# Kernel optimization log

Measured on AMD Instinct MI355X. Metric: run time of the kernel, lower is better.

Reference implementation:

```python
import jax, jax.numpy as jnp
import numpy as np

B, N, CI, CO = 2, 64, 32, 32  # batch, n points, Rs_in channels (j), Rs_out channels (i)


def setup_inputs() -> dict:
    key = jax.random.key(0)
    kf, kg, kw = jax.random.split(key, 3)
    features = jax.random.normal(kf, (B, N, N, CI), dtype=jnp.float32)
    geometry = jax.random.normal(kg, (B, N, 3), dtype=jnp.float32)
    # Continuous kernel parameters: linear map from relative vector (xyz) to 6*CO*CI kernel entries
    W = jax.random.normal(kw, (3, 6 * CO * CI), dtype=jnp.float32) / jnp.sqrt(3.0)
    return {"features": features, "geometry": geometry, "W": W, "n_norm": 1}


def reference(features, geometry, W, n_norm):
    z, n = geometry.shape[:2]
    ci = features.shape[-1]
    co = W.shape[1] // (6 * ci)
    # rel[z, a, b] = r_b - r_a  (rb = unsqueeze(1), ra = unsqueeze(2))
    rel = geometry[:, None, :, :] - geometry[:, :, None, :]  # [z, a, b, 3]
    k = jnp.einsum('zabx,xk->zabk', rel, W).reshape(z, n, n, 6 * co, ci)
    k = k / jnp.sqrt(6.0 * (n_norm ** 2))
    k1, k2, k3, k4, k5, k6 = jnp.split(k, 6, axis=3)  # each [z, a, b, i, j]
    # Precompute shared feature reductions over c and d once (fused HBM savings)
    fs = features.sum(axis=2)   # sum over d -> [z, c, j]
    fd = features.sum(axis=1)   # sum over c -> [z, d, j]
    ft = fs.sum(axis=1)         # sum over c,d -> [z, j]
    out = jnp.einsum('zabij,zj->zabi', k1, ft)
    out = out + jnp.einsum('zacij,zcj->zai', k2, fs)[:, :, None, :]
    out = out + jnp.einsum('zadij,zdj->zai', k3, fd)[:, :, None, :]
    out = out + jnp.einsum('zbcij,zcj->zbi', k4, fs)[:, None, :, :]
    out = out + jnp.einsum('zbdij,zdj->zbi', k5, fd)[:, None, :, :]
    out = out + jnp.einsum('zcdij,zcdj->zi', k6, features)[:, None, None, :]
    return out  # [z, a, b, i]
```

## Files before the change

### kernel.cpp

```cpp
#include <hip/hip_runtime.h>
#include <math.h>

#define NZ 2
#define NN 64
#define NCI 32
#define NCO 32
#define NBZ 32
#define NROWS (4096 / NBZ)

__device__ __forceinline__ void ld4(const float* __restrict__ p, float* d) {
    const float4 v = *(const float4*)p;
    d[0] = v.x; d[1] = v.y; d[2] = v.z; d[3] = v.w;
}

__global__ __launch_bounds__(256) void k_single(const float* __restrict__ feat,
                                                const float* __restrict__ geom,
                                                const float* __restrict__ W,
                                                const int* __restrict__ nnp,
                                                float* __restrict__ out) {
    const int bid = blockIdx.x;
    const int z   = bid >> 5;
    const int s   = bid & 31;
    const int tid = threadIdx.x;
    const int wv  = tid >> 6;
    const int lane = tid & 63;
    const int rg  = tid >> 3;
    const int cg  = tid & 7;

    __shared__ float gsh[NN * 3];
    __shared__ float wred[4][7][32];
    __shared__ float sacc[7][32];
    __shared__ float gred[3][32];
    __shared__ float stab[224];

    if (tid < NN * 3) gsh[tid] = geom[z * NN * 3 + tid];
    __syncthreads();

    float ft[4] = {0.f, 0.f, 0.f, 0.f};
    float Gs[3][4] = {{0.f}};
    float Gd[3][4] = {{0.f}};
    const float* fz = feat + (size_t)z * 4096 * NCI;
    #pragma unroll
    for (int rr = 0; rr < 2; ++rr) {
        const int c = rg * 2 + rr;
        const float gc0 = gsh[c * 3 + 0], gc1 = gsh[c * 3 + 1], gc2 = gsh[c * 3 + 2];
        const float* rowp = fz + (size_t)c * 64 * NCI + cg * 4;
        float rs[4] = {0.f, 0.f, 0.f, 0.f};
        #pragma unroll 4
        for (int d = 0; d < 64; ++d) {
            float f[4];
            ld4(rowp + d * NCI, f);
            const float gd0 = gsh[d * 3 + 0], gd1 = gsh[d * 3 + 1], gd2 = gsh[d * 3 + 2];
            #pragma unroll
            for (int k = 0; k < 4; ++k) {
                rs[k] += f[k];
                Gd[0][k] = fmaf(gd0, f[k], Gd[0][k]);
                Gd[1][k] = fmaf(gd1, f[k], Gd[1][k]);
                Gd[2][k] = fmaf(gd2, f[k], Gd[2][k]);
            }
        }
        #pragma unroll
        for (int k = 0; k < 4; ++k) {
            ft[k] += rs[k];
            Gs[0][k] = fmaf(gc0, rs[k], Gs[0][k]);
            Gs[1][k] = fmaf(gc1, rs[k], Gs[1][k]);
            Gs[2][k] = fmaf(gc2, rs[k], Gs[2][k]);
        }
    }

    float v[7][4];
    #pragma unroll
    for (int k = 0; k < 4; ++k) {
        v[0][k] = ft[k];
        #pragma unroll
        for (int x = 0; x < 3; ++x) { v[1 + x][k] = Gs[x][k]; v[4 + x][k] = Gd[x][k]; }
    }
    #pragma unroll
    for (int q = 0; q < 7; ++q)
        #pragma unroll
        for (int k = 0; k < 4; ++k) {
            float t = v[q][k];
            t += __shfl_xor(t, 8);
            t += __shfl_xor(t, 16);
            t += __shfl_xor(t, 32);
            v[q][k] = t;
        }
    if (lane < 8) {
        #pragma unroll
        for (int q = 0; q < 7; ++q)
            #pragma unroll
            for (int k = 0; k < 4; ++k) wred[wv][q][lane * 4 + k] = v[q][k];
    }
    __syncthreads();
    if (tid < 224) {
        const int q = tid >> 5, j = tid & 31;
        sacc[q][j] = wred[0][q][j] + wred[1][q][j] + wred[2][q][j] + wred[3][q][j];
    }
    __syncthreads();

    const int vn = *nnp;
    const float nnv = (vn > 0 && vn < (1 << 23)) ? (float)vn : __int_as_float(vn);
    const float scale = 1.0f / sqrtf(6.0f * nnv * nnv);

    if (tid < 96) {
        const int x = tid >> 5, i = tid & 31;
        const float* Wp = W + x * 6 * NCO * NCI + i * NCI;
        float q1 = 0.f, q23 = 0.f, q45 = 0.f, gp = 0.f;
        #pragma unroll 2
        for (int j4 = 0; j4 < 8; ++j4) {
            float w[6][4];
            #pragma unroll
            for (int m = 0; m < 6; ++m) ld4(Wp + m * 1024 + j4 * 4, w[m]);
            #pragma unroll
            for (int k = 0; k < 4; ++k) {
                const int j = j4 * 4 + k;
                const float ftj = sacc[0][j];
                const float gsj = sacc[1 + x][j];
                const float gdj = sacc[4 + x][j];
                q1  = fmaf(w[0][k], ftj, q1);
                q23 = fmaf(w[1][k] + w[2][k], ftj, q23);
                q45 = fmaf(w[3][k] + w[4][k], ftj, q45);
                gp  = fmaf(w[1][k] + w[3][k] - w[5][k], gsj, gp);
                gp  = fmaf(w[2][k] + w[4][k] + w[5][k], gdj, gp);
            }
        }
        stab[tid]      = scale * (q1 + q23);
        stab[96 + tid] = scale * (q1 - q45);
        gred[x][i] = gp;
    }
    __syncthreads();
    if (tid < 32) stab[192 + tid] = scale * (gred[0][tid] + gred[1][tid] + gred[2][tid]);
    __syncthreads();

    const int i0 = cg * 4;
    float qa[3][4], qb[3][4], gm[4];
    #pragma unroll
    for (int k = 0; k < 4; ++k) gm[k] = stab[192 + i0 + k];
    #pragma unroll
    for (int x = 0; x < 3; ++x)
        #pragma unroll
        for (int k = 0; k < 4; ++k) {
            qa[x][k] = stab[x * 32 + i0 + k];
            qb[x][k] = stab[96 + x * 32 + i0 + k];
        }

    #pragma unroll
    for (int u = 0; u < 4; ++u) {
        const int pr = rg + u * 32;
        const int ab = s * NROWS + pr;
        const int a = ab >> 6, b = ab & 63;
        float r[4];
        #pragma unroll
        for (int k = 0; k < 4; ++k) r[k] = gm[k];
        #pragma unroll
        for (int x = 0; x < 3; ++x) {
            const float gb = gsh[b * 3 + x], ga = gsh[a * 3 + x];
            #pragma unroll
            for (int k = 0; k < 4; ++k)
                r[k] = fmaf(gb, qb[x][k], fmaf(-ga, qa[x][k], r[k]));
        }
        float4 o; o.x = r[0]; o.y = r[1]; o.z = r[2]; o.w = r[3];
        *(float4*)(out + ((size_t)(z * 4096 + ab)) * 32 + i0) = o;
    }
}

extern "C" void kernel_launch(void* const* d_in, const int* in_sizes, int n_in,
                              void* d_out, int out_size, void* d_ws, size_t ws_size,
                              hipStream_t stream) {
    const float* feat = (const float*)d_in[0];
    const float* geom = (const float*)d_in[1];
    const float* W    = (const float*)d_in[2];
    const int*   nnp  = (const int*)d_in[3];

    k_single<<<NZ * NBZ, 256, 0, stream>>>(feat, geom, W, nnp, (float*)d_out);
}
```

Before: 16.81 us.

## Widen blocks to 1024 threads and redistribute reduction, weight and output work

Raises the block size from 256 to 1024 threads. Each thread now reduces half of one feature row, the W contraction is split across 8 lanes per output and combined with shuffles, and each thread writes one output vector instead of four. The goal is to shorten each thread's serial chain and expose more memory parallelism in a latency-bound redundant reduction that every block repeats. The cost is a larger 16-wave cross-wave reduction, more shuffles, and possibly lower occupancy or register pressure at 1024 threads per block.

```diff
diff --git a/kernel.cpp b/kernel.cpp
--- a/kernel.cpp
+++ b/kernel.cpp
@@ -6,29 +6,26 @@
 #define NCI 32
 #define NCO 32
 #define NBZ 32
-#define NROWS (4096 / NBZ)
 
 __device__ __forceinline__ void ld4(const float* __restrict__ p, float* d) {
     const float4 v = *(const float4*)p;
     d[0] = v.x; d[1] = v.y; d[2] = v.z; d[3] = v.w;
 }
 
-__global__ __launch_bounds__(256) void k_single(const float* __restrict__ feat,
-                                                const float* __restrict__ geom,
-                                                const float* __restrict__ W,
-                                                const int* __restrict__ nnp,
-                                                float* __restrict__ out) {
-    const int bid = blockIdx.x;
-    const int z   = bid >> 5;
-    const int s   = bid & 31;
-    const int tid = threadIdx.x;
-    const int wv  = tid >> 6;
+__global__ __launch_bounds__(1024) void k_single(const float* __restrict__ feat,
+                                                 const float* __restrict__ geom,
+                                                 const float* __restrict__ W,
+                                                 const int* __restrict__ nnp,
+                                                 float* __restrict__ out) {
+    const int bid  = blockIdx.x;
+    const int z    = bid >> 5;
+    const int s    = bid & 31;
+    const int tid  = threadIdx.x;
     const int lane = tid & 63;
-    const int rg  = tid >> 3;
-    const int cg  = tid & 7;
+    const int wv   = tid >> 6;
 
     __shared__ float gsh[NN * 3];
-    __shared__ float wred[4][7][32];
+    __shared__ float wred[16][7][32];
     __shared__ float sacc[7][32];
     __shared__ float gred[3][32];
     __shared__ float stab[224];
@@ -36,44 +33,35 @@
     if (tid < NN * 3) gsh[tid] = geom[z * NN * 3 + tid];
     __syncthreads();
 
-    float ft[4] = {0.f, 0.f, 0.f, 0.f};
-    float Gs[3][4] = {{0.f}};
+    const int cg = tid & 7;
+    const int dh = (tid >> 3) & 1;
+    const int c  = tid >> 4;
+    const float gc0 = gsh[c * 3 + 0], gc1 = gsh[c * 3 + 1], gc2 = gsh[c * 3 + 2];
+
+    float rs[4] = {0.f, 0.f, 0.f, 0.f};
     float Gd[3][4] = {{0.f}};
-    const float* fz = feat + (size_t)z * 4096 * NCI;
-    #pragma unroll
-    for (int rr = 0; rr < 2; ++rr) {
-        const int c = rg * 2 + rr;
-        const float gc0 = gsh[c * 3 + 0], gc1 = gsh[c * 3 + 1], gc2 = gsh[c * 3 + 2];
-        const float* rowp = fz + (size_t)c * 64 * NCI + cg * 4;
-        float rs[4] = {0.f, 0.f, 0.f, 0.f};
-        #pragma unroll 4
-        for (int d = 0; d < 64; ++d) {
-            float f[4];
-            ld4(rowp + d * NCI, f);
-            const float gd0 = gsh[d * 3 + 0], gd1 = gsh[d * 3 + 1], gd2 = gsh[d * 3 + 2];
-            #pragma unroll
-            for (int k = 0; k < 4; ++k) {
-                rs[k] += f[k];
-                Gd[0][k] = fmaf(gd0, f[k], Gd[0][k]);
-                Gd[1][k] = fmaf(gd1, f[k], Gd[1][k]);
-                Gd[2][k] = fmaf(gd2, f[k], Gd[2][k]);
-            }
-        }
+    const float* rowp = feat + ((size_t)z * 4096 + c * 64 + dh * 32) * NCI + cg * 4;
+    #pragma unroll 8
+    for (int t = 0; t < 32; ++t) {
+        float f[4];
+        ld4(rowp + t * NCI, f);
+        const int d = dh * 32 + t;
+        const float gd0 = gsh[d * 3 + 0], gd1 = gsh[d * 3 + 1], gd2 = gsh[d * 3 + 2];
         #pragma unroll
         for (int k = 0; k < 4; ++k) {
-            ft[k] += rs[k];
-            Gs[0][k] = fmaf(gc0, rs[k], Gs[0][k]);
-            Gs[1][k] = fmaf(gc1, rs[k], Gs[1][k]);
-            Gs[2][k] = fmaf(gc2, rs[k], Gs[2][k]);
+            rs[k] += f[k];
+            Gd[0][k] = fmaf(gd0, f[k], Gd[0][k]);
+            Gd[1][k] = fmaf(gd1, f[k], Gd[1][k]);
+            Gd[2][k] = fmaf(gd2, f[k], Gd[2][k]);
         }
     }
 
     float v[7][4];
     #pragma unroll
     for (int k = 0; k < 4; ++k) {
-        v[0][k] = ft[k];
-        #pragma unroll
-        for (int x = 0; x < 3; ++x) { v[1 + x][k] = Gs[x][k]; v[4 + x][k] = Gd[x][k]; }
+        v[0][k] = rs[k];
+        v[1][k] = gc0 * rs[k]; v[2][k] = gc1 * rs[k]; v[3][k] = gc2 * rs[k];
+        v[4][k] = Gd[0][k];    v[5][k] = Gd[1][k];    v[6][k] = Gd[2][k];
     }
     #pragma unroll
     for (int q = 0; q < 7; ++q)
@@ -94,7 +82,10 @@
     __syncthreads();
     if (tid < 224) {
         const int q = tid >> 5, j = tid & 31;
-        sacc[q][j] = wred[0][q][j] + wred[1][q][j] + wred[2][q][j] + wred[3][q][j];
+        float sum = 0.f;
+        #pragma unroll
+        for (int g = 0; g < 16; ++g) sum += wred[g][q][j];
+        sacc[q][j] = sum;
     }
     __syncthreads();
 
@@ -102,66 +93,59 @@
     const float nnv = (vn > 0 && vn < (1 << 23)) ? (float)vn : __int_as_float(vn);
     const float scale = 1.0f / sqrtf(6.0f * nnv * nnv);
 
-    if (tid < 96) {
-        const int x = tid >> 5, i = tid & 31;
-        const float* Wp = W + x * 6 * NCO * NCI + i * NCI;
+    if (tid < 768) {
+        const int x = tid >> 8, i = (tid >> 3) & 31, jg = tid & 7;
+        const float* Wp = W + x * 6 * NCO * NCI + i * NCI + jg * 4;
+        float w[6][4];
+        #pragma unroll
+        for (int m = 0; m < 6; ++m) ld4(Wp + m * 1024, w[m]);
         float q1 = 0.f, q23 = 0.f, q45 = 0.f, gp = 0.f;
-        #pragma unroll 2
-        for (int j4 = 0; j4 < 8; ++j4) {
-            float w[6][4];
-            #pragma unroll
-            for (int m = 0; m < 6; ++m) ld4(Wp + m * 1024 + j4 * 4, w[m]);
-            #pragma unroll
-            for (int k = 0; k < 4; ++k) {
-                const int j = j4 * 4 + k;
-                const float ftj = sacc[0][j];
-                const float gsj = sacc[1 + x][j];
-                const float gdj = sacc[4 + x][j];
-                q1  = fmaf(w[0][k], ftj, q1);
-                q23 = fmaf(w[1][k] + w[2][k], ftj, q23);
-                q45 = fmaf(w[3][k] + w[4][k], ftj, q45);
-                gp  = fmaf(w[1][k] + w[3][k] - w[5][k], gsj, gp);
-                gp  = fmaf(w[2][k] + w[4][k] + w[5][k], gdj, gp);
-            }
+        #pragma unroll
+        for (int k = 0; k < 4; ++k) {
+            const int j = jg * 4 + k;
+            const float ftj = sacc[0][j];
+            const float gsj = sacc[1 + x][j];
+            const float gdj = sacc[4 + x][j];
+            q1  = fmaf(w[0][k], ftj, q1);
+            q23 = fmaf(w[1][k] + w[2][k], ftj, q23);
+            q45 = fmaf(w[3][k] + w[4][k], ftj, q45);
+            gp  = fmaf(w[1][k] + w[3][k] - w[5][k], gsj, gp);
+            gp  = fmaf(w[2][k] + w[4][k] + w[5][k], gdj, gp);
         }
-        stab[tid]      = scale * (q1 + q23);
-        stab[96 + tid] = scale * (q1 - q45);
-        gred[x][i] = gp;
+        #pragma unroll
+        for (int m = 1; m <= 4; m <<= 1) {
+            q1  += __shfl_xor(q1, m);
+            q23 += __shfl_xor(q23, m);
+            q45 += __shfl_xor(q45, m);
+            gp  += __shfl_xor(gp, m);
+        }
+        if (jg == 0) {
+            stab[x * 32 + i]      = scale * (q1 + q23);
+            stab[96 + x * 32 + i] = scale * (q1 - q45);
+            gred[x][i] = gp;
+        }
     }
     __syncthreads();
     if (tid < 32) stab[192 + tid] = scale * (gred[0][tid] + gred[1][tid] + gred[2][tid]);
     __syncthreads();
 
+    const int r  = tid >> 3;
+    const int ab = s * 128 + r;
+    const int a = ab >> 6, b = ab & 63;
     const int i0 = cg * 4;
-    float qa[3][4], qb[3][4], gm[4];
+    float o4[4];
     #pragma unroll
-    for (int k = 0; k < 4; ++k) gm[k] = stab[192 + i0 + k];
+    for (int k = 0; k < 4; ++k) o4[k] = stab[192 + i0 + k];
     #pragma unroll
-    for (int x = 0; x < 3; ++x)
+    for (int x = 0; x < 3; ++x) {
+        const float gb = gsh[b * 3 + x], ga = gsh[a * 3 + x];
         #pragma unroll
-        for (int k = 0; k < 4; ++k) {
-            qa[x][k] = stab[x * 32 + i0 + k];
-            qb[x][k] = stab[96 + x * 32 + i0 + k];
-        }
-
-    #pragma unroll
-    for (int u = 0; u < 4; ++u) {
-        const int pr = rg + u * 32;
-        const int ab = s * NROWS + pr;
-        const int a = ab >> 6, b = ab & 63;
-        float r[4];
-        #pragma unroll
-        for (int k = 0; k < 4; ++k) r[k] = gm[k];
-        #pragma unroll
-        for (int x = 0; x < 3; ++x) {
-            const float gb = gsh[b * 3 + x], ga = gsh[a * 3 + x];
-            #pragma unroll
-            for (int k = 0; k < 4; ++k)
-                r[k] = fmaf(gb, qb[x][k], fmaf(-ga, qa[x][k], r[k]));
-        }
-        float4 o; o.x = r[0]; o.y = r[1]; o.z = r[2]; o.w = r[3];
-        *(float4*)(out + ((size_t)(z * 4096 + ab)) * 32 + i0) = o;
+        for (int k = 0; k < 4; ++k)
+            o4[k] = fmaf(gb, stab[96 + x * 32 + i0 + k],
+                         fmaf(-ga, stab[x * 32 + i0 + k], o4[k]));
     }
+    float4 o; o.x = o4[0]; o.y = o4[1]; o.z = o4[2]; o.w = o4[3];
+    *(float4*)(out + ((size_t)(z * 4096 + ab)) * NCI + i0) = o;
 }
 
 extern "C" void kernel_launch(void* const* d_in, const int* in_sizes, int n_in,
@@ -172,5 +156,5 @@
     const float* W    = (const float*)d_in[2];
     const int*   nnp  = (const int*)d_in[3];
 
-    k_single<<<NZ * NBZ, 256, 0, stream>>>(feat, geom, W, nnp, (float*)d_out);
+    k_single<<<NZ * NBZ, 1024, 0, stream>>>(feat, geom, W, nnp, (float*)d_out);
 }
```

Result: faster. 14.36 us, median of 2 (-14.6%).
